# Kernel tuning notes

Hardware: AMD Instinct MI355X
Metric: run time of the kernel (lower is better)

The kernel has to match this reference:

```python
import jax, jax.numpy as jnp
import numpy as np

MUL = 32           # multiplicity of each irrep (0e and 1e) in inputs and output
E = 50000          # number of edges
DIM = 4 * MUL      # 32x0e (32) + 32x1e (96) = 128

# e3nn FullyConnectedTensorProduct normalization (irrep_normalization='component',
# path_normalization='element'):
#   output 0e: paths (0e,0e->0e),(1e,1e->0e): alpha = dim(0e)/ (1024+1024) -> sqrt(1/2048)
#   output 1e: paths (0e,1e),(1e,0e),(1e,1e): alpha = dim(1e)/(3*1024)    -> sqrt(1/1024)
C_OUT0 = (1.0 / 2048.0) ** 0.5
C_OUT1 = (1.0 / 1024.0) ** 0.5
# real-basis Wigner 3j constants (e3nn conventions):
#   w3j(1,1,0) = delta_ij/sqrt(3); w3j(0,1,1)=w3j(1,0,1)=delta/sqrt(3); w3j(1,1,1)=eps_ijk/sqrt(6)
INV_SQRT3 = 3.0 ** -0.5
INV_SQRT6 = 6.0 ** -0.5


def _levi_civita():
    e = np.zeros((3, 3, 3), dtype=np.float32)
    e[0, 1, 2] = e[1, 2, 0] = e[2, 0, 1] = 1.0
    e[0, 2, 1] = e[2, 1, 0] = e[1, 0, 2] = -1.0
    return jnp.asarray(e)


def setup_inputs() -> dict:
    key = jax.random.key(0)
    ks = jax.random.split(key, 7)
    wshape = (MUL, MUL, MUL)  # uvw weights per path (e3nn init: standard normal)
    return {
        "x1": jax.random.normal(ks[0], (E, DIM), dtype=jnp.float32),
        "x2": jax.random.normal(ks[1], (E, DIM), dtype=jnp.float32),
        "W000": jax.random.normal(ks[2], wshape, dtype=jnp.float32),
        "W110": jax.random.normal(ks[3], wshape, dtype=jnp.float32),
        "W011": jax.random.normal(ks[4], wshape, dtype=jnp.float32),
        "W101": jax.random.normal(ks[5], wshape, dtype=jnp.float32),
        "W111": jax.random.normal(ks[6], wshape, dtype=jnp.float32),
    }


def reference(x1, x2, W000, W110, W011, W101, W111):
    # split irreps: [E, 32] scalars (0e), [E, 32, 3] vectors (1e), mul-major layout
    a0, a1 = x1[:, :MUL], x1[:, MUL:].reshape(-1, MUL, 3)
    b0, b1 = x2[:, :MUL], x2[:, MUL:].reshape(-1, MUL, 3)
    eps = _levi_civita()

    # scalar (0e) output: 0e x 0e -> 0e  and  1e . 1e -> 0e
    out0 = C_OUT0 * (
        jnp.einsum('uvw,eu,ev->ew', W000, a0, b0)
        + INV_SQRT3 * jnp.einsum('uvw,eui,evi->ew', W110, a1, b1)
    )

    # vector (1e) output: 0e*1e -> 1e, 1e*0e -> 1e, 1e x 1e -> 1e (cross product)
    out1 = C_OUT1 * (
        INV_SQRT3 * (
            jnp.einsum('uvw,eu,evk->ewk', W011, a0, b1)
            + jnp.einsum('uvw,euk,ev->ewk', W101, a1, b0)
        )
        + INV_SQRT6 * jnp.einsum('uvw,ijk,eui,evj->ewk', W111, eps, a1, b1)
    )

    return jnp.concatenate([out0, out1.reshape(-1, MUL * 3)], axis=1)  # [E, 128]
```

## Files before the change

### kernel.cpp

```cpp
#include <hip/hip_runtime.h>
#include <hip/hip_bf16.h>


typedef __attribute__((ext_vector_type(8))) short short8;
typedef __attribute__((ext_vector_type(4))) float f32x4;

static constexpr float C_OUT0    = 0.022097086912079608f;
static constexpr float C_OUT1    = 0.03125f;
static constexpr float INV_SQRT3 = 0.57735026918962576f;
static constexpr float INV_SQRT6 = 0.40824829046386302f;

static __device__ __forceinline__ short bfbits(float x) {
    __hip_bfloat16 h = __float2bfloat16(x);
    return __builtin_bit_cast(short, h);
}

__global__ __launch_bounds__(256) void prep_weights(
    const float* __restrict__ W000, const float* __restrict__ W110,
    const float* __restrict__ W011, const float* __restrict__ W101,
    const float* __restrict__ W111, short* __restrict__ wsB)
{
    const int t = blockIdx.x * 256 + threadIdx.x;
    if (t >= 5 * 32768) return;
    const int g   = t >> 15;
    const int idx = t & 32767;
    const int u = idx >> 10, v = (idx >> 5) & 31, w = idx & 31;
    const float* Wp = (g == 0) ? W000 : (g == 1) ? W110 : (g == 2) ? W011
                    : (g == 3) ? W101 : W111;
    const float s = (g == 0) ? C_OUT0
                  : (g == 1) ? C_OUT0 * INV_SQRT3
                  : (g == 4) ? C_OUT1 * INV_SQRT6
                  :            C_OUT1 * INV_SQRT3;
    const int f = 2 * g + (w >> 4);
    const int l = ((u >> 3) << 4) | (w & 15);
    const int j = u & 7;
    wsB[(((v * 10 + f) * 64) + l) * 8 + j] = bfbits(s * Wp[idx]);
}

__global__ __launch_bounds__(256) void e3nn_ts(
    const float* __restrict__ x1, const float* __restrict__ x2,
    const short8* __restrict__ wsB, float* __restrict__ out, int E)
{
    __shared__ __align__(16) float rawS[32 * 132];
    __shared__ __align__(16) float bT[128 * 36];
    float4* raw4 = (float4*)rawS;

    const int tid   = threadIdx.x;
    const int l     = tid & 63;
    const int wv    = tid >> 6;
    const int t     = wv & 1;
    const int vh    = wv >> 1;
    const int eBase = blockIdx.x * 32;

    const float4* x1v = (const float4*)x1;
    for (int i = tid; i < 32 * 32; i += 256) {
        const int e = i >> 5, c4 = i & 31;
        float4 val = {0.f, 0.f, 0.f, 0.f};
        if (eBase + e < E) val = x1v[(size_t)(eBase + e) * 32 + c4];
        raw4[e * 33 + c4] = val;
    }
    __syncthreads();

    const int eloc = l & 15;
    const int u0   = (l >> 4) * 8;
    {
        const float* row = rawS + (t * 16 + eloc) * 132;
    }
    short8 Aa0, Aax, Aay, Aaz;
    {
        const float* row = rawS + (t * 16 + eloc) * 132;
        #pragma unroll
        for (int j = 0; j < 8; ++j) {
            Aa0[j] = bfbits(row[u0 + j]);
            Aax[j] = bfbits(row[32 + 3 * (u0 + j) + 0]);
            Aay[j] = bfbits(row[32 + 3 * (u0 + j) + 1]);
            Aaz[j] = bfbits(row[32 + 3 * (u0 + j) + 2]);
        }
    }
    __syncthreads();

    const float4* x2v = (const float4*)x2;
    for (int i = tid; i < 32 * 32; i += 256) {
        const int e = i >> 5, c4 = i & 31;
        float4 val = {0.f, 0.f, 0.f, 0.f};
        if (eBase + e < E) val = x2v[(size_t)(eBase + e) * 32 + c4];
        raw4[e * 33 + c4] = val;
    }
    __syncthreads();

    {
        const int s  = tid >> 1;
        const int eh = tid & 1;
        const int v  = s >> 2, c = s & 3;
        const int r  = (c == 0) ? v : (32 + v * 3 + (c - 1));
        #pragma unroll
        for (int ee = 0; ee < 16; ++ee) {
            const int e = eh * 16 + ee;
            bT[s * 36 + e] = rawS[e * 132 + r];
        }
    }
    __syncthreads();

    const f32x4 zero = {0.f, 0.f, 0.f, 0.f};
    f32x4 acc0[2]    = {zero, zero};
    f32x4 acc1[3][2] = {{zero, zero}, {zero, zero}, {zero, zero}};

    const short8* wb  = wsB + l;
    const float*  bTt = bT + t * 16 + (l >> 4) * 4;

    #pragma unroll 2
    for (int v = vh * 16; v < vh * 16 + 16; ++v) {
        const short8* p = wb + v * 640;
        short8 Bf[10];
        #pragma unroll
        for (int f = 0; f < 10; ++f) Bf[f] = p[f * 64];

        const f32x4 B0 = *(const f32x4*)(bTt + (v * 4 + 0) * 36);
        const f32x4 Bx = *(const f32x4*)(bTt + (v * 4 + 1) * 36);
        const f32x4 By = *(const f32x4*)(bTt + (v * 4 + 2) * 36);
        const f32x4 Bz = *(const f32x4*)(bTt + (v * 4 + 3) * 36);

        #pragma unroll
        for (int nf = 0; nf < 2; ++nf) {
            const f32x4 G000  = __builtin_amdgcn_mfma_f32_16x16x32_bf16(Aa0, Bf[0 + nf], zero, 0, 0, 0);
            const f32x4 G110x = __builtin_amdgcn_mfma_f32_16x16x32_bf16(Aax, Bf[2 + nf], zero, 0, 0, 0);
            const f32x4 G110y = __builtin_amdgcn_mfma_f32_16x16x32_bf16(Aay, Bf[2 + nf], zero, 0, 0, 0);
            const f32x4 G110z = __builtin_amdgcn_mfma_f32_16x16x32_bf16(Aaz, Bf[2 + nf], zero, 0, 0, 0);
            acc0[nf] += B0 * G000 + Bx * G110x + By * G110y + Bz * G110z;

            const f32x4 G011  = __builtin_amdgcn_mfma_f32_16x16x32_bf16(Aa0, Bf[4 + nf], zero, 0, 0, 0);
            acc1[0][nf] += Bx * G011;
            acc1[1][nf] += By * G011;
            acc1[2][nf] += Bz * G011;

            const f32x4 G101x = __builtin_amdgcn_mfma_f32_16x16x32_bf16(Aax, Bf[6 + nf], zero, 0, 0, 0);
            const f32x4 G101y = __builtin_amdgcn_mfma_f32_16x16x32_bf16(Aay, Bf[6 + nf], zero, 0, 0, 0);
            const f32x4 G101z = __builtin_amdgcn_mfma_f32_16x16x32_bf16(Aaz, Bf[6 + nf], zero, 0, 0, 0);
            acc1[0][nf] += B0 * G101x;
            acc1[1][nf] += B0 * G101y;
            acc1[2][nf] += B0 * G101z;

            const f32x4 G111x = __builtin_amdgcn_mfma_f32_16x16x32_bf16(Aax, Bf[8 + nf], zero, 0, 0, 0);
            const f32x4 G111y = __builtin_amdgcn_mfma_f32_16x16x32_bf16(Aay, Bf[8 + nf], zero, 0, 0, 0);
            const f32x4 G111z = __builtin_amdgcn_mfma_f32_16x16x32_bf16(Aaz, Bf[8 + nf], zero, 0, 0, 0);
            acc1[0][nf] += Bz * G111y - By * G111z;
            acc1[1][nf] += Bx * G111z - Bz * G111x;
            acc1[2][nf] += By * G111x - Bx * G111y;
        }
    }

    __syncthreads();

    float* red = rawS;
    const int rbase = (t * 64 + l) * 33;
    if (vh == 1) {
        #pragma unroll
        for (int nf = 0; nf < 2; ++nf)
            #pragma unroll
            for (int r = 0; r < 4; ++r) {
                red[rbase + (0 + nf) * 4 + r] = acc0[nf][r];
                red[rbase + (2 + nf) * 4 + r] = acc1[0][nf][r];
                red[rbase + (4 + nf) * 4 + r] = acc1[1][nf][r];
                red[rbase + (6 + nf) * 4 + r] = acc1[2][nf][r];
            }
    }
    __syncthreads();

    if (vh == 0) {
        const int be0 = t * 16 + (l >> 4) * 4;
        #pragma unroll
        for (int nf = 0; nf < 2; ++nf) {
            const int w = nf * 16 + (l & 15);
            #pragma unroll
            for (int r = 0; r < 4; ++r) {
                const int ge = eBase + be0 + r;
                if (ge < E) {
                    const size_t base = (size_t)ge * 128;
                    out[base + w] =
                        acc0[nf][r] + red[rbase + (0 + nf) * 4 + r];
                    out[base + 32 + 3 * w + 0] =
                        acc1[0][nf][r] + red[rbase + (2 + nf) * 4 + r];
                    out[base + 32 + 3 * w + 1] =
                        acc1[1][nf][r] + red[rbase + (4 + nf) * 4 + r];
                    out[base + 32 + 3 * w + 2] =
                        acc1[2][nf][r] + red[rbase + (6 + nf) * 4 + r];
                }
            }
        }
    }
}

extern "C" void kernel_launch(void* const* d_in, const int* in_sizes, int n_in,
                              void* d_out, int out_size, void* d_ws, size_t ws_size,
                              hipStream_t stream) {
    const float* x1   = (const float*)d_in[0];
    const float* x2   = (const float*)d_in[1];
    const float* W000 = (const float*)d_in[2];
    const float* W110 = (const float*)d_in[3];
    const float* W011 = (const float*)d_in[4];
    const float* W101 = (const float*)d_in[5];
    const float* W111 = (const float*)d_in[6];
    float* out = (float*)d_out;

    const int E = in_sizes[0] / 128;

    hipLaunchKernelGGL(prep_weights, dim3((5 * 32768 + 255) / 256), dim3(256), 0, stream,
                       W000, W110, W011, W101, W111, (short*)d_ws);

    const int grid = (E + 31) / 32;
    hipLaunchKernelGGL(e3nn_ts, dim3(grid), dim3(256), 0, stream,
                       x1, x2, (const short8*)d_ws, out, E);
}
```

Before: 81.27 us.

## Split v-reduction across four waves with 16 edges per block

Each block now handles 16 edges instead of 32, and its four waves each take a quarter of the v range (8 values) over the same edges. Before, two edge-halves were each split across two v-halves. The partial accumulators are then summed serially through shared memory over three sync stages. This doubles the grid and shrinks shared memory per block, which should raise occupancy and parallelism. In exchange, every block reloads the full weight tensor for half as many edges, and the cross-wave reduction gets longer.

```diff
diff --git a/kernel.cpp b/kernel.cpp
--- a/kernel.cpp
+++ b/kernel.cpp
@@ -37,23 +37,21 @@
     wsB[(((v * 10 + f) * 64) + l) * 8 + j] = bfbits(s * Wp[idx]);
 }
 
-__global__ __launch_bounds__(256) void e3nn_ts(
+__global__ __launch_bounds__(256) void e3nn_q4(
     const float* __restrict__ x1, const float* __restrict__ x2,
     const short8* __restrict__ wsB, float* __restrict__ out, int E)
 {
-    __shared__ __align__(16) float rawS[32 * 132];
-    __shared__ __align__(16) float bT[128 * 36];
+    __shared__ __align__(16) float rawS[16 * 132];
+    __shared__ __align__(16) float bT[128 * 20];
     float4* raw4 = (float4*)rawS;
 
     const int tid   = threadIdx.x;
     const int l     = tid & 63;
-    const int wv    = tid >> 6;
-    const int t     = wv & 1;
-    const int vh    = wv >> 1;
-    const int eBase = blockIdx.x * 32;
+    const int vq    = tid >> 6;
+    const int eBase = blockIdx.x * 16;
 
     const float4* x1v = (const float4*)x1;
-    for (int i = tid; i < 32 * 32; i += 256) {
+    for (int i = tid; i < 16 * 32; i += 256) {
         const int e = i >> 5, c4 = i & 31;
         float4 val = {0.f, 0.f, 0.f, 0.f};
         if (eBase + e < E) val = x1v[(size_t)(eBase + e) * 32 + c4];
@@ -63,12 +61,9 @@
 
     const int eloc = l & 15;
     const int u0   = (l >> 4) * 8;
-    {
-        const float* row = rawS + (t * 16 + eloc) * 132;
-    }
     short8 Aa0, Aax, Aay, Aaz;
     {
-        const float* row = rawS + (t * 16 + eloc) * 132;
+        const float* row = rawS + eloc * 132;
         #pragma unroll
         for (int j = 0; j < 8; ++j) {
             Aa0[j] = bfbits(row[u0 + j]);
@@ -80,7 +75,7 @@
     __syncthreads();
 
     const float4* x2v = (const float4*)x2;
-    for (int i = tid; i < 32 * 32; i += 256) {
+    for (int i = tid; i < 16 * 32; i += 256) {
         const int e = i >> 5, c4 = i & 31;
         float4 val = {0.f, 0.f, 0.f, 0.f};
         if (eBase + e < E) val = x2v[(size_t)(eBase + e) * 32 + c4];
@@ -94,9 +89,9 @@
         const int v  = s >> 2, c = s & 3;
         const int r  = (c == 0) ? v : (32 + v * 3 + (c - 1));
         #pragma unroll
-        for (int ee = 0; ee < 16; ++ee) {
-            const int e = eh * 16 + ee;
-            bT[s * 36 + e] = rawS[e * 132 + r];
+        for (int k = 0; k < 8; ++k) {
+            const int e = eh * 8 + k;
+            bT[s * 20 + e] = rawS[e * 132 + r];
         }
     }
     __syncthreads();
@@ -106,19 +101,19 @@
     f32x4 acc1[3][2] = {{zero, zero}, {zero, zero}, {zero, zero}};
 
     const short8* wb  = wsB + l;
-    const float*  bTt = bT + t * 16 + (l >> 4) * 4;
+    const float*  bTt = bT + (l >> 4) * 4;
 
     #pragma unroll 2
-    for (int v = vh * 16; v < vh * 16 + 16; ++v) {
+    for (int v = vq * 8; v < vq * 8 + 8; ++v) {
         const short8* p = wb + v * 640;
         short8 Bf[10];
         #pragma unroll
         for (int f = 0; f < 10; ++f) Bf[f] = p[f * 64];
 
-        const f32x4 B0 = *(const f32x4*)(bTt + (v * 4 + 0) * 36);
-        const f32x4 Bx = *(const f32x4*)(bTt + (v * 4 + 1) * 36);
-        const f32x4 By = *(const f32x4*)(bTt + (v * 4 + 2) * 36);
-        const f32x4 Bz = *(const f32x4*)(bTt + (v * 4 + 3) * 36);
+        const f32x4 B0 = *(const f32x4*)(bTt + (v * 4 + 0) * 20);
+        const f32x4 Bx = *(const f32x4*)(bTt + (v * 4 + 1) * 20);
+        const f32x4 By = *(const f32x4*)(bTt + (v * 4 + 2) * 20);
+        const f32x4 Bz = *(const f32x4*)(bTt + (v * 4 + 3) * 20);
 
         #pragma unroll
         for (int nf = 0; nf < 2; ++nf) {
@@ -149,11 +144,11 @@
         }
     }
 
-    __syncthreads();
-
     float* red = rawS;
-    const int rbase = (t * 64 + l) * 33;
-    if (vh == 1) {
+    const int rbase = l * 33;
+
+    __syncthreads();
+    if (vq == 3) {
         #pragma unroll
         for (int nf = 0; nf < 2; ++nf)
             #pragma unroll
@@ -165,9 +160,33 @@
             }
     }
     __syncthreads();
-
-    if (vh == 0) {
-        const int be0 = t * 16 + (l >> 4) * 4;
+    if (vq == 2) {
+        #pragma unroll
+        for (int nf = 0; nf < 2; ++nf)
+            #pragma unroll
+            for (int r = 0; r < 4; ++r) {
+                red[rbase + (0 + nf) * 4 + r] += acc0[nf][r];
+                red[rbase + (2 + nf) * 4 + r] += acc1[0][nf][r];
+                red[rbase + (4 + nf) * 4 + r] += acc1[1][nf][r];
+                red[rbase + (6 + nf) * 4 + r] += acc1[2][nf][r];
+            }
+    }
+    __syncthreads();
+    if (vq == 1) {
+        #pragma unroll
+        for (int nf = 0; nf < 2; ++nf)
+            #pragma unroll
+            for (int r = 0; r < 4; ++r) {
+                red[rbase + (0 + nf) * 4 + r] += acc0[nf][r];
+                red[rbase + (2 + nf) * 4 + r] += acc1[0][nf][r];
+                red[rbase + (4 + nf) * 4 + r] += acc1[1][nf][r];
+                red[rbase + (6 + nf) * 4 + r] += acc1[2][nf][r];
+            }
+    }
+    __syncthreads();
+
+    if (vq == 0) {
+        const int be0 = (l >> 4) * 4;
         #pragma unroll
         for (int nf = 0; nf < 2; ++nf) {
             const int w = nf * 16 + (l & 15);
@@ -207,7 +226,7 @@
     hipLaunchKernelGGL(prep_weights, dim3((5 * 32768 + 255) / 256), dim3(256), 0, stream,
                        W000, W110, W011, W101, W111, (short*)d_ws);
 
-    const int grid = (E + 31) / 32;
-    hipLaunchKernelGGL(e3nn_ts, dim3(grid), dim3(256), 0, stream,
+    const int grid = (E + 15) / 16;
+    hipLaunchKernelGGL(e3nn_q4, dim3(grid), dim3(256), 0, stream,
                        x1, x2, (const short8*)d_ws, out, E);
 }
```

Result: no change. 79.71 us (-1.9%).

## Split v-loop across four waves with each wave covering both edge tiles

Applied to the files above, without the earlier changes.

Each wave now processes both 16-edge tiles and a quarter of the v range, instead of one edge tile and half the v range. Each weight fragment loaded from global/L2 is reused for two edge tiles, halving weight-load traffic per MFMA. The cost is doubled accumulator and A-fragment registers, which may lower occupancy, plus a longer serial three-stage shared-memory reduction across the four waves.

```diff
diff --git a/kernel.cpp b/kernel.cpp
--- a/kernel.cpp
+++ b/kernel.cpp
@@ -37,7 +37,7 @@
     wsB[(((v * 10 + f) * 64) + l) * 8 + j] = bfbits(s * Wp[idx]);
 }
 
-__global__ __launch_bounds__(256) void e3nn_ts(
+__global__ __launch_bounds__(256) void e3nn_2t(
     const float* __restrict__ x1, const float* __restrict__ x2,
     const short8* __restrict__ wsB, float* __restrict__ out, int E)
 {
@@ -47,9 +47,7 @@
 
     const int tid   = threadIdx.x;
     const int l     = tid & 63;
-    const int wv    = tid >> 6;
-    const int t     = wv & 1;
-    const int vh    = wv >> 1;
+    const int vq    = tid >> 6;
     const int eBase = blockIdx.x * 32;
 
     const float4* x1v = (const float4*)x1;
@@ -63,18 +61,16 @@
 
     const int eloc = l & 15;
     const int u0   = (l >> 4) * 8;
-    {
+    short8 Aa0[2], Aax[2], Aay[2], Aaz[2];
+    #pragma unroll
+    for (int t = 0; t < 2; ++t) {
         const float* row = rawS + (t * 16 + eloc) * 132;
-    }
-    short8 Aa0, Aax, Aay, Aaz;
-    {
-        const float* row = rawS + (t * 16 + eloc) * 132;
         #pragma unroll
         for (int j = 0; j < 8; ++j) {
-            Aa0[j] = bfbits(row[u0 + j]);
-            Aax[j] = bfbits(row[32 + 3 * (u0 + j) + 0]);
-            Aay[j] = bfbits(row[32 + 3 * (u0 + j) + 1]);
-            Aaz[j] = bfbits(row[32 + 3 * (u0 + j) + 2]);
+            Aa0[t][j] = bfbits(row[u0 + j]);
+            Aax[t][j] = bfbits(row[32 + 3 * (u0 + j) + 0]);
+            Aay[t][j] = bfbits(row[32 + 3 * (u0 + j) + 1]);
+            Aaz[t][j] = bfbits(row[32 + 3 * (u0 + j) + 2]);
         }
     }
     __syncthreads();
@@ -102,88 +98,138 @@
     __syncthreads();
 
     const f32x4 zero = {0.f, 0.f, 0.f, 0.f};
-    f32x4 acc0[2]    = {zero, zero};
-    f32x4 acc1[3][2] = {{zero, zero}, {zero, zero}, {zero, zero}};
+    f32x4 acc0[2][2];
+    f32x4 acc1[2][3][2];
+    #pragma unroll
+    for (int t = 0; t < 2; ++t) {
+        acc0[t][0] = zero; acc0[t][1] = zero;
+        #pragma unroll
+        for (int k = 0; k < 3; ++k) { acc1[t][k][0] = zero; acc1[t][k][1] = zero; }
+    }
 
     const short8* wb  = wsB + l;
-    const float*  bTt = bT + t * 16 + (l >> 4) * 4;
-
-    #pragma unroll 2
-    for (int v = vh * 16; v < vh * 16 + 16; ++v) {
+    const int     goff = (l >> 4) * 4;
+
+    for (int v = vq * 8; v < vq * 8 + 8; ++v) {
         const short8* p = wb + v * 640;
         short8 Bf[10];
         #pragma unroll
         for (int f = 0; f < 10; ++f) Bf[f] = p[f * 64];
 
-        const f32x4 B0 = *(const f32x4*)(bTt + (v * 4 + 0) * 36);
-        const f32x4 Bx = *(const f32x4*)(bTt + (v * 4 + 1) * 36);
-        const f32x4 By = *(const f32x4*)(bTt + (v * 4 + 2) * 36);
-        const f32x4 Bz = *(const f32x4*)(bTt + (v * 4 + 3) * 36);
-
-        #pragma unroll
-        for (int nf = 0; nf < 2; ++nf) {
-            const f32x4 G000  = __builtin_amdgcn_mfma_f32_16x16x32_bf16(Aa0, Bf[0 + nf], zero, 0, 0, 0);
-            const f32x4 G110x = __builtin_amdgcn_mfma_f32_16x16x32_bf16(Aax, Bf[2 + nf], zero, 0, 0, 0);
-            const f32x4 G110y = __builtin_amdgcn_mfma_f32_16x16x32_bf16(Aay, Bf[2 + nf], zero, 0, 0, 0);
-            const f32x4 G110z = __builtin_amdgcn_mfma_f32_16x16x32_bf16(Aaz, Bf[2 + nf], zero, 0, 0, 0);
-            acc0[nf] += B0 * G000 + Bx * G110x + By * G110y + Bz * G110z;
-
-            const f32x4 G011  = __builtin_amdgcn_mfma_f32_16x16x32_bf16(Aa0, Bf[4 + nf], zero, 0, 0, 0);
-            acc1[0][nf] += Bx * G011;
-            acc1[1][nf] += By * G011;
-            acc1[2][nf] += Bz * G011;
-
-            const f32x4 G101x = __builtin_amdgcn_mfma_f32_16x16x32_bf16(Aax, Bf[6 + nf], zero, 0, 0, 0);
-            const f32x4 G101y = __builtin_amdgcn_mfma_f32_16x16x32_bf16(Aay, Bf[6 + nf], zero, 0, 0, 0);
-            const f32x4 G101z = __builtin_amdgcn_mfma_f32_16x16x32_bf16(Aaz, Bf[6 + nf], zero, 0, 0, 0);
-            acc1[0][nf] += B0 * G101x;
-            acc1[1][nf] += B0 * G101y;
-            acc1[2][nf] += B0 * G101z;
-
-            const f32x4 G111x = __builtin_amdgcn_mfma_f32_16x16x32_bf16(Aax, Bf[8 + nf], zero, 0, 0, 0);
-            const f32x4 G111y = __builtin_amdgcn_mfma_f32_16x16x32_bf16(Aay, Bf[8 + nf], zero, 0, 0, 0);
-            const f32x4 G111z = __builtin_amdgcn_mfma_f32_16x16x32_bf16(Aaz, Bf[8 + nf], zero, 0, 0, 0);
-            acc1[0][nf] += Bz * G111y - By * G111z;
-            acc1[1][nf] += Bx * G111z - Bz * G111x;
-            acc1[2][nf] += By * G111x - Bx * G111y;
-        }
-    }
-
-    __syncthreads();
+        #pragma unroll
+        for (int t = 0; t < 2; ++t) {
+            const float* bTt = bT + t * 16 + goff;
+            const f32x4 B0 = *(const f32x4*)(bTt + (v * 4 + 0) * 36);
+            const f32x4 Bx = *(const f32x4*)(bTt + (v * 4 + 1) * 36);
+            const f32x4 By = *(const f32x4*)(bTt + (v * 4 + 2) * 36);
+            const f32x4 Bz = *(const f32x4*)(bTt + (v * 4 + 3) * 36);
+
+            #pragma unroll
+            for (int nf = 0; nf < 2; ++nf) {
+                const f32x4 G000  = __builtin_amdgcn_mfma_f32_16x16x32_bf16(Aa0[t], Bf[0 + nf], zero, 0, 0, 0);
+                const f32x4 G110x = __builtin_amdgcn_mfma_f32_16x16x32_bf16(Aax[t], Bf[2 + nf], zero, 0, 0, 0);
+                const f32x4 G110y = __builtin_amdgcn_mfma_f32_16x16x32_bf16(Aay[t], Bf[2 + nf], zero, 0, 0, 0);
+                const f32x4 G110z = __builtin_amdgcn_mfma_f32_16x16x32_bf16(Aaz[t], Bf[2 + nf], zero, 0, 0, 0);
+                acc0[t][nf] += B0 * G000 + Bx * G110x + By * G110y + Bz * G110z;
+
+                const f32x4 G011  = __builtin_amdgcn_mfma_f32_16x16x32_bf16(Aa0[t], Bf[4 + nf], zero, 0, 0, 0);
+                acc1[t][0][nf] += Bx * G011;
+                acc1[t][1][nf] += By * G011;
+                acc1[t][2][nf] += Bz * G011;
+
+                const f32x4 G101x = __builtin_amdgcn_mfma_f32_16x16x32_bf16(Aax[t], Bf[6 + nf], zero, 0, 0, 0);
+                const f32x4 G101y = __builtin_amdgcn_mfma_f32_16x16x32_bf16(Aay[t], Bf[6 + nf], zero, 0, 0, 0);
+                const f32x4 G101z = __builtin_amdgcn_mfma_f32_16x16x32_bf16(Aaz[t], Bf[6 + nf], zero, 0, 0, 0);
+                acc1[t][0][nf] += B0 * G101x;
+                acc1[t][1][nf] += B0 * G101y;
+                acc1[t][2][nf] += B0 * G101z;
+
+                const f32x4 G111x = __builtin_amdgcn_mfma_f32_16x16x32_bf16(Aax[t], Bf[8 + nf], zero, 0, 0, 0);
+                const f32x4 G111y = __builtin_amdgcn_mfma_f32_16x16x32_bf16(Aay[t], Bf[8 + nf], zero, 0, 0, 0);
+                const f32x4 G111z = __builtin_amdgcn_mfma_f32_16x16x32_bf16(Aaz[t], Bf[8 + nf], zero, 0, 0, 0);
+                acc1[t][0][nf] += Bz * G111y - By * G111z;
+                acc1[t][1][nf] += Bx * G111z - Bz * G111x;
+                acc1[t][2][nf] += By * G111x - Bx * G111y;
+            }
+        }
+    }
 
     float* red = rawS;
-    const int rbase = (t * 64 + l) * 33;
-    if (vh == 1) {
-        #pragma unroll
-        for (int nf = 0; nf < 2; ++nf)
-            #pragma unroll
-            for (int r = 0; r < 4; ++r) {
-                red[rbase + (0 + nf) * 4 + r] = acc0[nf][r];
-                red[rbase + (2 + nf) * 4 + r] = acc1[0][nf][r];
-                red[rbase + (4 + nf) * 4 + r] = acc1[1][nf][r];
-                red[rbase + (6 + nf) * 4 + r] = acc1[2][nf][r];
-            }
-    }
-    __syncthreads();
-
-    if (vh == 0) {
-        const int be0 = t * 16 + (l >> 4) * 4;
-        #pragma unroll
-        for (int nf = 0; nf < 2; ++nf) {
-            const int w = nf * 16 + (l & 15);
-            #pragma unroll
-            for (int r = 0; r < 4; ++r) {
-                const int ge = eBase + be0 + r;
-                if (ge < E) {
-                    const size_t base = (size_t)ge * 128;
-                    out[base + w] =
-                        acc0[nf][r] + red[rbase + (0 + nf) * 4 + r];
-                    out[base + 32 + 3 * w + 0] =
-                        acc1[0][nf][r] + red[rbase + (2 + nf) * 4 + r];
-                    out[base + 32 + 3 * w + 1] =
-                        acc1[1][nf][r] + red[rbase + (4 + nf) * 4 + r];
-                    out[base + 32 + 3 * w + 2] =
-                        acc1[2][nf][r] + red[rbase + (6 + nf) * 4 + r];
+    const int rb0 = l * 33;
+    const int rb1 = (64 + l) * 33;
+
+    __syncthreads();
+    if (vq == 3) {
+        #pragma unroll
+        for (int t = 0; t < 2; ++t) {
+            const int rb = t ? rb1 : rb0;
+            #pragma unroll
+            for (int nf = 0; nf < 2; ++nf)
+                #pragma unroll
+                for (int r = 0; r < 4; ++r) {
+                    red[rb + (0 + nf) * 4 + r] = acc0[t][nf][r];
+                    red[rb + (2 + nf) * 4 + r] = acc1[t][0][nf][r];
+                    red[rb + (4 + nf) * 4 + r] = acc1[t][1][nf][r];
+                    red[rb + (6 + nf) * 4 + r] = acc1[t][2][nf][r];
+                }
+        }
+    }
+    __syncthreads();
+    if (vq == 2) {
+        #pragma unroll
+        for (int t = 0; t < 2; ++t) {
+            const int rb = t ? rb1 : rb0;
+            #pragma unroll
+            for (int nf = 0; nf < 2; ++nf)
+                #pragma unroll
+                for (int r = 0; r < 4; ++r) {
+                    red[rb + (0 + nf) * 4 + r] += acc0[t][nf][r];
+                    red[rb + (2 + nf) * 4 + r] += acc1[t][0][nf][r];
+                    red[rb + (4 + nf) * 4 + r] += acc1[t][1][nf][r];
+                    red[rb + (6 + nf) * 4 + r] += acc1[t][2][nf][r];
+                }
+        }
+    }
+    __syncthreads();
+    if (vq == 1) {
+        #pragma unroll
+        for (int t = 0; t < 2; ++t) {
+            const int rb = t ? rb1 : rb0;
+            #pragma unroll
+            for (int nf = 0; nf < 2; ++nf)
+                #pragma unroll
+                for (int r = 0; r < 4; ++r) {
+                    red[rb + (0 + nf) * 4 + r] += acc0[t][nf][r];
+                    red[rb + (2 + nf) * 4 + r] += acc1[t][0][nf][r];
+                    red[rb + (4 + nf) * 4 + r] += acc1[t][1][nf][r];
+                    red[rb + (6 + nf) * 4 + r] += acc1[t][2][nf][r];
+                }
+        }
+    }
+    __syncthreads();
+
+    if (vq == 0) {
+        #pragma unroll
+        for (int t = 0; t < 2; ++t) {
+            const int rb  = t ? rb1 : rb0;
+            const int be0 = t * 16 + goff;
+            #pragma unroll
+            for (int nf = 0; nf < 2; ++nf) {
+                const int w = nf * 16 + (l & 15);
+                #pragma unroll
+                for (int r = 0; r < 4; ++r) {
+                    const int ge = eBase + be0 + r;
+                    if (ge < E) {
+                        const size_t base = (size_t)ge * 128;
+                        out[base + w] =
+                            acc0[t][nf][r] + red[rb + (0 + nf) * 4 + r];
+                        out[base + 32 + 3 * w + 0] =
+                            acc1[t][0][nf][r] + red[rb + (2 + nf) * 4 + r];
+                        out[base + 32 + 3 * w + 1] =
+                            acc1[t][1][nf][r] + red[rb + (4 + nf) * 4 + r];
+                        out[base + 32 + 3 * w + 2] =
+                            acc1[t][2][nf][r] + red[rb + (6 + nf) * 4 + r];
+                    }
                 }
             }
         }
@@ -208,6 +254,6 @@
                        W000, W110, W011, W101, W111, (short*)d_ws);
 
     const int grid = (E + 31) / 32;
-    hipLaunchKernelGGL(e3nn_ts, dim3(grid), dim3(256), 0, stream,
+    hipLaunchKernelGGL(e3nn_2t, dim3(grid), dim3(256), 0, stream,
                        x1, x2, (const short8*)d_ws, out, E);
 }
```

Measured after the change: 85.54 us. 5.3% more time.
